# Kernel tuning notes

Hardware: AMD Instinct MI355X
Metric: run time of the kernel (lower is better)

Reference implementation:

```python
import jax, jax.numpy as jnp
import numpy as np

TOP_K = 2
LN_EPS = 1e-5
GATE_EPS = 1e-6


def setup_inputs() -> dict:
    key = jax.random.key(0)
    ks = jax.random.split(key, 5)
    B, D, E, H, O = 16384, 1200, 8, 1024, 1
    x = jax.random.normal(ks[0], (B, D), dtype=jnp.float32)
    w_gate = jax.random.normal(ks[1], (D, E), dtype=jnp.float32) * 0.05
    W1 = jax.random.normal(ks[2], (E, D, H), dtype=jnp.float32) * (1.0 / np.sqrt(D))
    b1 = jnp.zeros((E, H), dtype=jnp.float32)
    g1 = jnp.ones((E, H), dtype=jnp.float32)   # LayerNorm weight
    be1 = jnp.zeros((E, H), dtype=jnp.float32)  # LayerNorm bias
    W2 = jax.random.normal(ks[3], (E, H, O), dtype=jnp.float32) * (1.0 / np.sqrt(H))
    b2 = jnp.zeros((E, O), dtype=jnp.float32)
    return {"x": x, "w_gate": w_gate, "W1": W1, "b1": b1, "g1": g1, "be1": be1, "W2": W2, "b2": b2}


def reference(x, w_gate, W1, b1, g1, be1, W2, b2):
    B = x.shape[0]
    # --- top-k gating (eval mode: no noise) ---
    probs = jax.nn.softmax(x @ w_gate, axis=1)                 # [B, E]
    top_vals, top_idx = jax.lax.top_k(probs, TOP_K)            # [B, k]
    top_gates = top_vals / (jnp.sum(top_vals, axis=1, keepdims=True) + GATE_EPS)
    gates = jnp.zeros_like(probs).at[jnp.arange(B)[:, None], top_idx].set(top_gates)  # [B, E]
    # --- per-expert MLP (computed densely for all experts; gates zero out non-selected) ---
    h = jnp.einsum('bd,edh->beh', x, W1) + b1                  # [B, E, H]
    mu = jnp.mean(h, axis=-1, keepdims=True)
    var = jnp.var(h, axis=-1, keepdims=True)
    h = (h - mu) * jax.lax.rsqrt(var + LN_EPS) * g1 + be1      # LayerNorm
    h = jax.nn.relu(h)
    out = jax.nn.sigmoid(jnp.einsum('beh,eho->beo', h, W2) + b2)  # [B, E, O]
    # --- scatter/combine: weighted sum over experts ---
    y = jnp.einsum('be,beo->bo', gates, out)                   # [B, O]
    return y
```

## Files before the change

### kernel.cpp

```cpp
#include <hip/hip_runtime.h>
#include <hip/hip_bf16.h>
#include <stdint.h>

#define B_ROWS 16384
#define D_IN   1200
#define D_PAD  1216
#define N_EXP  8
#define H_DIM  1024
#define CAP    33792
#define N_TILES 264
#define LN_EPS 1e-5f
#define GATE_EPS 1e-6f
#define CNT_STRIDE 16

#define O_CNT    0
#define O_POFF   512
#define O_CNT2   576
#define O_TOPI   1088
#define O_TOPG   132160
#define O_PROWC  263232
#define O_PGATEC 398400
#define O_XBF    533568
#define O_W1T    40381888
#define O_HBUF   60304832

#define GATING_BLOCKS (B_ROWS / 32)
#define W1T_BLOCKS    (19 * 16 * 8)

typedef short bf16x8 __attribute__((ext_vector_type(8)));
typedef short short8 __attribute__((ext_vector_type(8)));
typedef short short4v __attribute__((ext_vector_type(4)));
typedef float f32x4 __attribute__((ext_vector_type(4)));

__device__ __forceinline__ void load_lds16(const void* gptr, void* ldsptr) {
    __builtin_amdgcn_global_load_lds(
        (__attribute__((address_space(1))) void*)const_cast<void*>(gptr),
        (__attribute__((address_space(3))) void*)ldsptr, 16, 0, 0);
}

__device__ __forceinline__ short4v pack_bf16x4(float4 a) {
    union { short4v v; __hip_bfloat16 h[4]; } u;
    u.h[0] = __float2bfloat16(a.x); u.h[1] = __float2bfloat16(a.y);
    u.h[2] = __float2bfloat16(a.z); u.h[3] = __float2bfloat16(a.w);
    return u.v;
}

__global__ __launch_bounds__(256) void gating_w1t_kernel(
    const float* __restrict__ x, const float* __restrict__ wg,
    const float* __restrict__ W1,
    int* __restrict__ topIdx, float* __restrict__ topGate,
    int* __restrict__ cnt,
    __hip_bfloat16* __restrict__ w1t, __hip_bfloat16* __restrict__ xbf)
{
    __shared__ float tile[2][32][33];
    __shared__ int lhist[N_EXP];
    int bx = blockIdx.x;
    int tid = threadIdx.x;

    if (bx < GATING_BLOCKS) {
        if (tid < N_EXP) lhist[tid] = 0;
        __syncthreads();

        int widx = tid >> 6;
        int lane = tid & 63;
        int rowbase = bx * 32 + widx * 8;
        const float* xw = x + (long)rowbase * D_IN;

        float acc[8][8];
#pragma unroll
        for (int r = 0; r < 8; ++r)
#pragma unroll
            for (int e = 0; e < N_EXP; ++e) acc[r][e] = 0.f;

        for (int i = lane; i < 304; i += 64) {
            if (i < 300) {
                const float4* wv4 = (const float4*)(wg + (long)i * 32);
                float4 w0 = wv4[0], w1v = wv4[1], w2 = wv4[2], w3 = wv4[3],
                       w4 = wv4[4], w5 = wv4[5], w6 = wv4[6], w7 = wv4[7];
#pragma unroll
                for (int r = 0; r < 8; ++r) {
                    float4 xv = ((const float4*)(xw + (long)r * D_IN))[i];
                    acc[r][0] += xv.x * w0.x + xv.y * w2.x + xv.z * w4.x + xv.w * w6.x;
                    acc[r][1] += xv.x * w0.y + xv.y * w2.y + xv.z * w4.y + xv.w * w6.y;
                    acc[r][2] += xv.x * w0.z + xv.y * w2.z + xv.z * w4.z + xv.w * w6.z;
                    acc[r][3] += xv.x * w0.w + xv.y * w2.w + xv.z * w4.w + xv.w * w6.w;
                    acc[r][4] += xv.x * w1v.x + xv.y * w3.x + xv.z * w5.x + xv.w * w7.x;
                    acc[r][5] += xv.x * w1v.y + xv.y * w3.y + xv.z * w5.y + xv.w * w7.y;
                    acc[r][6] += xv.x * w1v.z + xv.y * w3.z + xv.z * w5.z + xv.w * w7.z;
                    acc[r][7] += xv.x * w1v.w + xv.y * w3.w + xv.z * w5.w + xv.w * w7.w;
                    ((short4v*)(xbf + (long)(rowbase + r) * D_PAD))[i] = pack_bf16x4(xv);
                }
            } else {
#pragma unroll
                for (int r = 0; r < 8; ++r)
                    ((short4v*)(xbf + (long)(rowbase + r) * D_PAD))[i] = (short4v){0, 0, 0, 0};
            }
        }

#pragma unroll
        for (int r = 0; r < 8; ++r)
#pragma unroll
            for (int e = 0; e < N_EXP; ++e) {
                float v = acc[r][e];
#pragma unroll
                for (int off = 32; off > 0; off >>= 1) v += __shfl_xor(v, off, 64);
                acc[r][e] = v;
            }

        float my[N_EXP];
#pragma unroll
        for (int e = 0; e < N_EXP; ++e) my[e] = acc[0][e];
#pragma unroll
        for (int r = 1; r < 8; ++r)
#pragma unroll
            for (int e = 0; e < N_EXP; ++e)
                if (lane == r) my[e] = acc[r][e];

        if (lane < 8) {
            float m = my[0];
#pragma unroll
            for (int e = 1; e < N_EXP; ++e) m = fmaxf(m, my[e]);
            float p[N_EXP], s = 0.f;
#pragma unroll
            for (int e = 0; e < N_EXP; ++e) { p[e] = expf(my[e] - m); s += p[e]; }
            int i0 = 0;
#pragma unroll
            for (int e = 1; e < N_EXP; ++e) if (p[e] > p[i0]) i0 = e;
            int i1 = (i0 == 0) ? 1 : 0;
#pragma unroll
            for (int e = 0; e < N_EXP; ++e) if (e != i0 && p[e] > p[i1]) i1 = e;
            float v0 = p[i0] / s, v1 = p[i1] / s;
            float inv = 1.f / (v0 + v1 + GATE_EPS);
            int row = rowbase + lane;
            ((int2*)topIdx)[row] = make_int2(i0, i1);
            ((float2*)topGate)[row] = make_float2(v0 * inv, v1 * inv);
            atomicAdd(&lhist[i0], 1);
            atomicAdd(&lhist[i1], 1);
        }
        __syncthreads();
        if (tid < N_EXP) atomicAdd(&cnt[tid * CNT_STRIDE], lhist[tid]);
    } else if (bx == GATING_BLOCKS) {
        short8* xrow = (short8*)(xbf + (long)B_ROWS * D_PAD);
        if (tid < 152) xrow[tid] = (short8){0, 0, 0, 0, 0, 0, 0, 0};
    } else {
        int b = bx - GATING_BLOCKS - 1;
        int d0 = (b % 19) * 64;
        int h0 = ((b / 19) % 16) * 64;
        int e = b / (19 * 16);
        const float* src = W1 + (long)e * D_IN * H_DIM;

        int hs = tid & 15;
        int dr = tid >> 4;
#pragma unroll
        for (int s = 0; s < 4; ++s) {
            int dl = dr + 16 * s;
            int d = d0 + dl;
            float4 v = (d < D_IN)
                ? ((const float4*)(src + (long)d * H_DIM + h0))[hs]
                : (float4){0.f, 0.f, 0.f, 0.f};
            int drl = dl & 31;
            int hl = hs * 4;
            int Th = hl >> 5;
            int hh = hl & 31;
            tile[Th][drl][hh + 0] = v.x;
            tile[Th][drl][hh + 1] = v.y;
            tile[Th][drl][hh + 2] = v.z;
            tile[Th][drl][hh + 3] = v.w;
            if (s == 1) {
                __syncthreads();
                int T2 = tid >> 7, rr = tid & 127;
                int hl2 = rr >> 2, dseg = rr & 3;
                float f[8];
#pragma unroll
                for (int j = 0; j < 8; ++j) f[j] = tile[T2][dseg * 8 + j][hl2];
                union { short8 v8; __hip_bfloat16 hh8[8]; } u;
#pragma unroll
                for (int j = 0; j < 8; ++j) u.hh8[j] = __float2bfloat16(f[j]);
                int h = h0 + T2 * 32 + hl2;
                ((short8*)(w1t + (long)e * H_DIM * D_PAD + (long)h * D_PAD + d0))[dseg] = u.v8;
                __syncthreads();
            }
        }
        __syncthreads();
        {
            int T2 = tid >> 7, rr = tid & 127;
            int hl2 = rr >> 2, dseg = rr & 3;
            float f[8];
#pragma unroll
            for (int j = 0; j < 8; ++j) f[j] = tile[T2][dseg * 8 + j][hl2];
            union { short8 v8; __hip_bfloat16 hh8[8]; } u;
#pragma unroll
            for (int j = 0; j < 8; ++j) u.hh8[j] = __float2bfloat16(f[j]);
            int h = h0 + T2 * 32 + hl2;
            ((short8*)(w1t + (long)e * H_DIM * D_PAD + (long)h * D_PAD + d0 + 32))[dseg] = u.v8;
        }
    }
}

__global__ void offsets_kernel(const int* __restrict__ cnt, int* __restrict__ poff)
{
    if (threadIdx.x == 0 && blockIdx.x == 0) {
        int o = 0;
        for (int e = 0; e < N_EXP; ++e) {
            poff[e] = o;
            o += (cnt[e * CNT_STRIDE] + 127) & ~127;
        }
        poff[N_EXP] = o;
    }
}

__global__ __launch_bounds__(256) void scatter_kernel(
    const int* __restrict__ topIdx, const float* __restrict__ topGate,
    const int* __restrict__ cnt, const int* __restrict__ poff, int* __restrict__ cnt2,
    int* __restrict__ pairRowC, float* __restrict__ pairGateC, float* __restrict__ y)
{
    int tid = threadIdx.x;
    int b = blockIdx.x;

    {
        int p = b * 256 + tid;
        int e = 0;
        while (e < N_EXP - 1 && p >= poff[e + 1]) ++e;
        if (p - poff[e] >= cnt[e * CNT_STRIDE]) {
            pairRowC[p] = B_ROWS;
            pairGateC[p] = 0.f;
        }
    }
    if (b >= B_ROWS / 256) return;

    int row = b * 256 + tid;
    y[row] = 0.f;

    __shared__ int lcnt[N_EXP];
    __shared__ int base[N_EXP];
    if (tid < N_EXP) lcnt[tid] = 0;
    __syncthreads();
    int2 e = ((const int2*)topIdx)[row];
    float2 g = ((const float2*)topGate)[row];
    int s0 = atomicAdd(&lcnt[e.x], 1);
    int s1 = atomicAdd(&lcnt[e.y], 1);
    __syncthreads();
    if (tid < N_EXP) base[tid] = atomicAdd(&cnt2[tid * CNT_STRIDE], lcnt[tid]);
    __syncthreads();
    int p0 = poff[e.x] + base[e.x] + s0;
    pairRowC[p0] = row; pairGateC[p0] = g.x;
    int p1 = poff[e.y] + base[e.y] + s1;
    pairRowC[p1] = row; pairGateC[p1] = g.y;
}

__global__ __launch_bounds__(256) void gemm_kernel(
    const __hip_bfloat16* __restrict__ xbf, const __hip_bfloat16* __restrict__ w1t,
    const float* __restrict__ b1, const int* __restrict__ poff,
    const int* __restrict__ pairRowC,
    __hip_bfloat16* __restrict__ hbuf)
{
    int bi = blockIdx.x;
    int xcd = bi & 7;
    int j = bi >> 3;
    int col0 = (j & 7) << 7;
    int rt = xcd * 33 + (j >> 3);
    int row0 = rt << 7;
    if (row0 >= poff[N_EXP]) return;
    int e = 0;
    while (e < N_EXP - 1 && row0 >= poff[e + 1]) ++e;

    __shared__ short lA[2][128 * 32];
    __shared__ short lB[2][128 * 32];

    int t = threadIdx.x;
    int lane = t & 63, w = t >> 6;
    int wm = (w >> 1) * 64, wn = (w & 1) * 64;
    int l15 = lane & 15, quad = lane >> 4;
    int qsw = quad ^ ((l15 >> 1) & 3);

    f32x4 acc[4][4];
#pragma unroll
    for (int i = 0; i < 4; ++i)
#pragma unroll
        for (int j2 = 0; j2 < 4; ++j2) acc[i][j2] = (f32x4){0.f, 0.f, 0.f, 0.f};

    int r1 = t >> 2, seg = t & 3;
    int sw = seg ^ ((r1 >> 1) & 3);
    int ridx1 = pairRowC[row0 + r1];
    int ridx2 = pairRowC[row0 + 64 + r1];
    const __hip_bfloat16* Arow1 = xbf + (long)ridx1 * D_PAD + sw * 8;
    const __hip_bfloat16* Arow2 = xbf + (long)ridx2 * D_PAD + sw * 8;
    const __hip_bfloat16* Bb = w1t + (long)e * H_DIM * D_PAD + (long)col0 * D_PAD;
    const __hip_bfloat16* Brow1 = Bb + (long)r1 * D_PAD + sw * 8;
    const __hip_bfloat16* Brow2 = Bb + (long)(r1 + 64) * D_PAD + sw * 8;

    for (int kt = 0; kt < D_PAD / 64; ++kt) {
        __syncthreads();
        int k0 = kt * 64;
        load_lds16(Arow1 + k0,      (char*)lA[0] + t * 16);
        load_lds16(Arow2 + k0,      (char*)lA[0] + t * 16 + 4096);
        load_lds16(Arow1 + k0 + 32, (char*)lA[1] + t * 16);
        load_lds16(Arow2 + k0 + 32, (char*)lA[1] + t * 16 + 4096);
        load_lds16(Brow1 + k0,      (char*)lB[0] + t * 16);
        load_lds16(Brow2 + k0,      (char*)lB[0] + t * 16 + 4096);
        load_lds16(Brow1 + k0 + 32, (char*)lB[1] + t * 16);
        load_lds16(Brow2 + k0 + 32, (char*)lB[1] + t * 16 + 4096);
        __syncthreads();

#pragma unroll
        for (int p = 0; p < 2; ++p) {
            const char* lAc = (const char*)lA[p];
            const char* lBc = (const char*)lB[p];
            bf16x8 af[4], bfr[4];
#pragma unroll
            for (int i = 0; i < 4; ++i)
                af[i] = *(const bf16x8*)(lAc + (wm + i * 16 + l15) * 64 + qsw * 16);
#pragma unroll
            for (int j2 = 0; j2 < 4; ++j2)
                bfr[j2] = *(const bf16x8*)(lBc + (wn + j2 * 16 + l15) * 64 + qsw * 16);
#pragma unroll
            for (int i = 0; i < 4; ++i)
#pragma unroll
                for (int j2 = 0; j2 < 4; ++j2)
                    acc[i][j2] = __builtin_amdgcn_mfma_f32_16x16x32_bf16(af[i], bfr[j2], acc[i][j2], 0, 0, 0);
        }
    }

#pragma unroll
    for (int i = 0; i < 4; ++i) {
        int lr = wm + i * 16 + quad * 4;
#pragma unroll
        for (int j2 = 0; j2 < 4; ++j2) {
            int gc = col0 + wn + j2 * 16 + l15;
            float bias = b1[e * H_DIM + gc];
#pragma unroll
            for (int r = 0; r < 4; ++r) {
                float v = acc[i][j2][r] + bias;
                hbuf[(long)(row0 + lr + r) * H_DIM + gc] = __float2bfloat16(v);
            }
        }
    }
}

__global__ __launch_bounds__(256) void ln_head_kernel(
    const __hip_bfloat16* __restrict__ hbuf, const int* __restrict__ cnt, const int* __restrict__ poff,
    const int* __restrict__ pairRowC, const float* __restrict__ pairGateC,
    const float* __restrict__ g1, const float* __restrict__ be1,
    const float* __restrict__ W2, const float* __restrict__ b2,
    float* __restrict__ y)
{
    int tid = threadIdx.x;
    int p = blockIdx.x * 4 + (tid >> 6);
    if (p >= poff[N_EXP]) return;
    int e = 0;
    while (e < N_EXP - 1 && p >= poff[e + 1]) ++e;
    if (p - poff[e] >= cnt[e * CNT_STRIDE]) return;

    int lane = tid & 63;
    int row = pairRowC[p];
    float gate = pairGateC[p];
    const short4v* hr = (const short4v*)(hbuf + (long)p * H_DIM);

    float v[16];
    float sum = 0.f, sumsq = 0.f;
#pragma unroll
    for (int k = 0; k < 4; ++k) {
        union { short4v s; __hip_bfloat16 h[4]; } hv;
        hv.s = hr[lane + k * 64];
#pragma unroll
        for (int j = 0; j < 4; ++j) {
            float f = __bfloat162float(hv.h[j]);
            v[k * 4 + j] = f;
            sum += f;
            sumsq += f * f;
        }
    }
#pragma unroll
    for (int off = 32; off > 0; off >>= 1) {
        sum += __shfl_xor(sum, off, 64);
        sumsq += __shfl_xor(sumsq, off, 64);
    }
    float mu = sum * (1.f / H_DIM);
    float var = sumsq * (1.f / H_DIM) - mu * mu;
    float rstd = rsqrtf(var + LN_EPS);

    float z = 0.f;
#pragma unroll
    for (int k = 0; k < 4; ++k) {
        float4 gv = ((const float4*)(g1 + e * H_DIM))[lane + k * 64];
        float4 bv = ((const float4*)(be1 + e * H_DIM))[lane + k * 64];
        float4 wv = ((const float4*)(W2 + e * H_DIM))[lane + k * 64];
        z += fmaxf((v[k*4+0] - mu) * rstd * gv.x + bv.x, 0.f) * wv.x;
        z += fmaxf((v[k*4+1] - mu) * rstd * gv.y + bv.y, 0.f) * wv.y;
        z += fmaxf((v[k*4+2] - mu) * rstd * gv.z + bv.z, 0.f) * wv.z;
        z += fmaxf((v[k*4+3] - mu) * rstd * gv.w + bv.w, 0.f) * wv.w;
    }
#pragma unroll
    for (int off = 32; off > 0; off >>= 1) z += __shfl_xor(z, off, 64);
    if (lane == 0) {
        float zt = z + b2[e];
        float o = 1.f / (1.f + expf(-zt));
        atomicAdd(&y[row], gate * o);
    }
}

extern "C" void kernel_launch(void* const* d_in, const int* in_sizes, int n_in,
                              void* d_out, int out_size, void* d_ws, size_t ws_size,
                              hipStream_t stream)
{
    const float* x   = (const float*)d_in[0];
    const float* wg  = (const float*)d_in[1];
    const float* W1  = (const float*)d_in[2];
    const float* b1  = (const float*)d_in[3];
    const float* g1  = (const float*)d_in[4];
    const float* be1 = (const float*)d_in[5];
    const float* W2  = (const float*)d_in[6];
    const float* b2  = (const float*)d_in[7];
    float* y = (float*)d_out;

    char* ws = (char*)d_ws;
    int*   cnt       = (int*)(ws + O_CNT);
    int*   poff      = (int*)(ws + O_POFF);
    int*   cnt2      = (int*)(ws + O_CNT2);
    int*   topIdx    = (int*)(ws + O_TOPI);
    float* topGate   = (float*)(ws + O_TOPG);
    int*   pairRowC  = (int*)(ws + O_PROWC);
    float* pairGateC = (float*)(ws + O_PGATEC);
    __hip_bfloat16* xbf  = (__hip_bfloat16*)(ws + O_XBF);
    __hip_bfloat16* w1t  = (__hip_bfloat16*)(ws + O_W1T);
    __hip_bfloat16* hbuf = (__hip_bfloat16*)(ws + O_HBUF);

    hipMemsetAsync(ws, 0, 1088, stream);

    gating_w1t_kernel<<<GATING_BLOCKS + 1 + W1T_BLOCKS, 256, 0, stream>>>(
        x, wg, W1, topIdx, topGate, cnt, w1t, xbf);
    offsets_kernel<<<1, 64, 0, stream>>>(cnt, poff);
    scatter_kernel<<<CAP / 256, 256, 0, stream>>>(topIdx, topGate, cnt, poff, cnt2,
                                                  pairRowC, pairGateC, y);
    gemm_kernel<<<N_TILES * 8, 256, 0, stream>>>(xbf, w1t, b1, poff, pairRowC, hbuf);
    ln_head_kernel<<<(CAP + 3) / 4, 256, 0, stream>>>(hbuf, cnt, poff, pairRowC, pairGateC,
                                                      g1, be1, W2, b2, y);
}
```

Measured before the change: 315.3 us.

## Enlarge GEMM tile to 256x128 with 512 threads and K-step 32

The grouped GEMM now uses 256-row by 128-column tiles computed by 8 waves (512 threads) instead of 128x128 tiles with 4 waves. Expert segments are padded to multiples of 256, and the capacity and workspace offsets are resized to match. Each K iteration now loads 32 columns instead of 64, which keeps LDS small. The aim is more reuse of each B tile and fewer blocks, at the cost of twice as many barriers per K range and more padded rows.

```diff
diff --git a/kernel.cpp b/kernel.cpp
--- a/kernel.cpp
+++ b/kernel.cpp
@@ -7,8 +7,8 @@
 #define D_PAD  1216
 #define N_EXP  8
 #define H_DIM  1024
-#define CAP    33792
-#define N_TILES 264
+#define CAP    34816
+#define N_RT   136
 #define LN_EPS 1e-5f
 #define GATE_EPS 1e-6f
 #define CNT_STRIDE 16
@@ -19,10 +19,10 @@
 #define O_TOPI   1088
 #define O_TOPG   132160
 #define O_PROWC  263232
-#define O_PGATEC 398400
-#define O_XBF    533568
-#define O_W1T    40381888
-#define O_HBUF   60304832
+#define O_PGATEC 402496
+#define O_XBF    541760
+#define O_W1T    40390080
+#define O_HBUF   60313024
 
 #define GATING_BLOCKS (B_ROWS / 32)
 #define W1T_BLOCKS    (19 * 16 * 8)
@@ -203,7 +203,7 @@
         int o = 0;
         for (int e = 0; e < N_EXP; ++e) {
             poff[e] = o;
-            o += (cnt[e * CNT_STRIDE] + 127) & ~127;
+            o += (cnt[e * CNT_STRIDE] + 255) & ~255;
         }
         poff[N_EXP] = o;
     }
@@ -248,7 +248,7 @@
     pairRowC[p1] = row; pairGateC[p1] = g.y;
 }
 
-__global__ __launch_bounds__(256) void gemm_kernel(
+__global__ __launch_bounds__(512) void gemm_kernel(
     const __hip_bfloat16* __restrict__ xbf, const __hip_bfloat16* __restrict__ w1t,
     const float* __restrict__ b1, const int* __restrict__ poff,
     const int* __restrict__ pairRowC,
@@ -258,18 +258,19 @@
     int xcd = bi & 7;
     int j = bi >> 3;
     int col0 = (j & 7) << 7;
-    int rt = xcd * 33 + (j >> 3);
-    int row0 = rt << 7;
+    int rt = xcd * 17 + (j >> 3);
+    int row0 = rt << 8;
     if (row0 >= poff[N_EXP]) return;
     int e = 0;
     while (e < N_EXP - 1 && row0 >= poff[e + 1]) ++e;
 
-    __shared__ short lA[2][128 * 32];
-    __shared__ short lB[2][128 * 32];
+    __shared__ short lA[256 * 32];
+    __shared__ short lB[128 * 32];
 
     int t = threadIdx.x;
     int lane = t & 63, w = t >> 6;
-    int wm = (w >> 1) * 64, wn = (w & 1) * 64;
+    int wm = (w >> 1) * 64;
+    int wn = (w & 1) * 64;
     int l15 = lane & 15, quad = lane >> 4;
     int qsw = quad ^ ((l15 >> 1) & 3);
 
@@ -282,43 +283,33 @@
     int r1 = t >> 2, seg = t & 3;
     int sw = seg ^ ((r1 >> 1) & 3);
     int ridx1 = pairRowC[row0 + r1];
-    int ridx2 = pairRowC[row0 + 64 + r1];
+    int ridx2 = pairRowC[row0 + 128 + r1];
     const __hip_bfloat16* Arow1 = xbf + (long)ridx1 * D_PAD + sw * 8;
     const __hip_bfloat16* Arow2 = xbf + (long)ridx2 * D_PAD + sw * 8;
-    const __hip_bfloat16* Bb = w1t + (long)e * H_DIM * D_PAD + (long)col0 * D_PAD;
-    const __hip_bfloat16* Brow1 = Bb + (long)r1 * D_PAD + sw * 8;
-    const __hip_bfloat16* Brow2 = Bb + (long)(r1 + 64) * D_PAD + sw * 8;
-
-    for (int kt = 0; kt < D_PAD / 64; ++kt) {
+    const __hip_bfloat16* Brow1 = w1t + (long)e * H_DIM * D_PAD + (long)(col0 + r1) * D_PAD + sw * 8;
+    char* lAc = (char*)lA;
+    char* lBc = (char*)lB;
+
+    for (int kt = 0; kt < D_PAD / 32; ++kt) {
         __syncthreads();
-        int k0 = kt * 64;
-        load_lds16(Arow1 + k0,      (char*)lA[0] + t * 16);
-        load_lds16(Arow2 + k0,      (char*)lA[0] + t * 16 + 4096);
-        load_lds16(Arow1 + k0 + 32, (char*)lA[1] + t * 16);
-        load_lds16(Arow2 + k0 + 32, (char*)lA[1] + t * 16 + 4096);
-        load_lds16(Brow1 + k0,      (char*)lB[0] + t * 16);
-        load_lds16(Brow2 + k0,      (char*)lB[0] + t * 16 + 4096);
-        load_lds16(Brow1 + k0 + 32, (char*)lB[1] + t * 16);
-        load_lds16(Brow2 + k0 + 32, (char*)lB[1] + t * 16 + 4096);
+        int k0 = kt * 32;
+        load_lds16(Arow1 + k0, lAc + t * 16);
+        load_lds16(Arow2 + k0, lAc + t * 16 + 8192);
+        load_lds16(Brow1 + k0, lBc + t * 16);
         __syncthreads();
 
-#pragma unroll
-        for (int p = 0; p < 2; ++p) {
-            const char* lAc = (const char*)lA[p];
-            const char* lBc = (const char*)lB[p];
-            bf16x8 af[4], bfr[4];
-#pragma unroll
-            for (int i = 0; i < 4; ++i)
-                af[i] = *(const bf16x8*)(lAc + (wm + i * 16 + l15) * 64 + qsw * 16);
+        bf16x8 af[4], bfr[4];
+#pragma unroll
+        for (int i = 0; i < 4; ++i)
+            af[i] = *(const bf16x8*)(lAc + (wm + i * 16 + l15) * 64 + qsw * 16);
+#pragma unroll
+        for (int j2 = 0; j2 < 4; ++j2)
+            bfr[j2] = *(const bf16x8*)(lBc + (wn + j2 * 16 + l15) * 64 + qsw * 16);
+#pragma unroll
+        for (int i = 0; i < 4; ++i)
 #pragma unroll
             for (int j2 = 0; j2 < 4; ++j2)
-                bfr[j2] = *(const bf16x8*)(lBc + (wn + j2 * 16 + l15) * 64 + qsw * 16);
-#pragma unroll
-            for (int i = 0; i < 4; ++i)
-#pragma unroll
-                for (int j2 = 0; j2 < 4; ++j2)
-                    acc[i][j2] = __builtin_amdgcn_mfma_f32_16x16x32_bf16(af[i], bfr[j2], acc[i][j2], 0, 0, 0);
-        }
+                acc[i][j2] = __builtin_amdgcn_mfma_f32_16x16x32_bf16(af[i], bfr[j2], acc[i][j2], 0, 0, 0);
     }
 
 #pragma unroll
@@ -432,7 +423,7 @@
     offsets_kernel<<<1, 64, 0, stream>>>(cnt, poff);
     scatter_kernel<<<CAP / 256, 256, 0, stream>>>(topIdx, topGate, cnt, poff, cnt2,
                                                   pairRowC, pairGateC, y);
-    gemm_kernel<<<N_TILES * 8, 256, 0, stream>>>(xbf, w1t, b1, poff, pairRowC, hbuf);
+    gemm_kernel<<<N_RT * 8, 512, 0, stream>>>(xbf, w1t, b1, poff, pairRowC, hbuf);
     ln_head_kernel<<<(CAP + 3) / 4, 256, 0, stream>>>(hbuf, cnt, poff, pairRowC, pairGateC,
                                                       g1, be1, W2, b2, y);
 }
```

New measurement: 313.0 us. No clear change (-0.7%).
